# Kernel tuning notes

Measured on AMD Instinct MI355X. Metric: run time of the kernel, lower is better.

The kernel has to match this reference:

```python
import jax, jax.numpy as jnp
import numpy as np

B, N, H_DIM, G_DIM, G_HID, K_CONST = 32, 8192, 256, 256, 512, 64


def setup_inputs() -> dict:
    key = jax.random.key(0)
    k1, k2, k3 = jax.random.split(key, 3)
    hs = jax.random.normal(k1, (B, N, H_DIM), dtype=jnp.float32)
    # Sorted cluster labels 0..K-1, same row for all batch entries (training mode).
    cs_row = ((jnp.arange(N) * K_CONST) // N).astype(jnp.int32)
    cs_o = jnp.tile(cs_row[None, :], (B, 1))
    W1 = jax.random.normal(k2, (H_DIM, G_HID), dtype=jnp.float32) * (1.0 / np.sqrt(H_DIM))
    b1 = jnp.zeros((G_HID,), dtype=jnp.float32)
    W2 = jax.random.normal(k3, (G_HID, G_DIM), dtype=jnp.float32) * (1.0 / np.sqrt(G_HID))
    b2 = jnp.zeros((G_DIM,), dtype=jnp.float32)
    return {"hs": hs, "cs_o": cs_o, "W1": W1, "b1": b1, "W2": W2, "b2": b2,
            "n": N - 1, "K": K_CONST}


def reference(hs, cs_o, W1, b1, W2, b2, n, K):
    # Training mode (cs_is_sample=False): mask points >= n, use row 0 pattern.
    cs = cs_o.at[:, n:].set(-1)
    cs1 = cs[0]  # [N]
    # One-hot cluster membership: [K, N]
    onehot = (cs1[None, :] == jnp.arange(K)[:, None]).astype(hs.dtype)
    # Per-cluster sums H_k: [B, K, h_dim] (single pass, replaces K masked sweeps)
    Hk = jnp.einsum('kn,bnh->bkh', onehot, hs)
    hn = hs[:, n, :]  # [B, h_dim]
    # H = [H_0..H_{K-1}, H_0+h_n..H_{K-1}+h_n, h_n] -> [B, 2K+1, h_dim]
    H = jnp.concatenate([Hk, Hk + hn[:, None, :], hn[:, None, :]], axis=1)
    # g: 2-layer MLP applied rowwise
    gs = jax.nn.relu(H @ W1 + b1) @ W2 + b2  # [B, 2K+1, g_dim]
    # Exclude-sum combine: G[:,k] = sum_{j<K} gs[:,j] - gs[:,k] + gs[:,k+K]
    S = gs[:, :K, :].sum(axis=1)  # [B, g_dim]
    G_front = S[:, None, :] - gs[:, :K, :] + gs[:, K:2 * K, :]
    G_last = (S + gs[:, 2 * K, :])[:, None, :]
    G = jnp.concatenate([G_front, G_last], axis=1)  # [B, K+1, g_dim]
    G_mask = jnp.ones((hs.shape[0], K + 1), dtype=hs.dtype)
    return G, G_mask
```

## Files before the change

### kernel.cpp

```cpp
#include <hip/hip_runtime.h>

#define B_SZ   32
#define N_SZ   8192
#define HDIM   256
#define GHID   512
#define K_CL   64
#define M_ROWS (B_SZ * (2 * K_CL + 1))
#define M_PAD  4224

typedef short v8s __attribute__((ext_vector_type(8)));
typedef float v4f __attribute__((ext_vector_type(4)));

__device__ __forceinline__ unsigned short f32_to_bf16(float f) {
  unsigned int u = __float_as_uint(f);
  u += 0x7FFFu + ((u >> 16) & 1u);
  return (unsigned short)(u >> 16);
}

__device__ __forceinline__ int lower_bound_i(const int* __restrict__ a, int n, int key) {
  int lo = 0, hi = n;
  while (lo < hi) {
    const int mid = (lo + hi) >> 1;
    if (a[mid] < key) lo = mid + 1; else hi = mid;
  }
  return lo;
}

__global__ __launch_bounds__(256) void cluster_sum_kernel(
    const float* __restrict__ hs, const int* __restrict__ cs,
    const int* __restrict__ n_ptr, float* __restrict__ Hk) {
  const int b = blockIdx.x;
  const int k = blockIdx.y;
  const int tid = threadIdx.x;
  const int col = (tid & 63) * 4;
  const int rsub = tid >> 6;
  const int n_val = n_ptr[0];

  const int start = lower_bound_i(cs, N_SZ, k);
  int end = lower_bound_i(cs, N_SZ, k + 1);
  if (end > n_val) end = n_val;

  const float* base = hs + (size_t)b * N_SZ * HDIM + col;

  float4 a0 = make_float4(0.f, 0.f, 0.f, 0.f), a1 = a0, a2 = a0, a3 = a0;
  int r = start + rsub;
  for (; r + 12 < end; r += 16) {
    const float4 v0 = *(const float4*)(base + (size_t)(r) * HDIM);
    const float4 v1 = *(const float4*)(base + (size_t)(r + 4) * HDIM);
    const float4 v2 = *(const float4*)(base + (size_t)(r + 8) * HDIM);
    const float4 v3 = *(const float4*)(base + (size_t)(r + 12) * HDIM);
    a0.x += v0.x; a0.y += v0.y; a0.z += v0.z; a0.w += v0.w;
    a1.x += v1.x; a1.y += v1.y; a1.z += v1.z; a1.w += v1.w;
    a2.x += v2.x; a2.y += v2.y; a2.z += v2.z; a2.w += v2.w;
    a3.x += v3.x; a3.y += v3.y; a3.z += v3.z; a3.w += v3.w;
  }
  for (; r < end; r += 4) {
    const float4 v = *(const float4*)(base + (size_t)r * HDIM);
    a0.x += v.x; a0.y += v.y; a0.z += v.z; a0.w += v.w;
  }
  float4 acc;
  acc.x = (a0.x + a1.x) + (a2.x + a3.x);
  acc.y = (a0.y + a1.y) + (a2.y + a3.y);
  acc.z = (a0.z + a1.z) + (a2.z + a3.z);
  acc.w = (a0.w + a1.w) + (a2.w + a3.w);

  __shared__ float4 red[256];
  red[tid] = acc;
  __syncthreads();
  if (tid < 64) {
    const float4 p0 = red[tid], p1 = red[tid + 64], p2 = red[tid + 128], p3 = red[tid + 192];
    float4 o;
    o.x = (p0.x + p1.x) + (p2.x + p3.x);
    o.y = (p0.y + p1.y) + (p2.y + p3.y);
    o.z = (p0.z + p1.z) + (p2.z + p3.z);
    o.w = (p0.w + p1.w) + (p2.w + p3.w);
    *(float4*)(Hk + ((size_t)b * K_CL + k) * HDIM + tid * 4) = o;
  }
}

__global__ __launch_bounds__(256) void prep_w_kernel(
    const float* __restrict__ W1, const float* __restrict__ W2,
    unsigned short* __restrict__ W1t, unsigned short* __restrict__ W2t) {
  const int idx = blockIdx.x;
  const int tid = threadIdx.x;
  __shared__ float tile[32][33];

  if (idx < 128) {
    const int tr = idx >> 4, tc = idx & 15;
    const int r0 = tid >> 5, c = tid & 31;
#pragma unroll
    for (int p = 0; p < 4; ++p) {
      const int r = p * 8 + r0;
      tile[r][c] = W1[(size_t)(tr * 32 + r) * GHID + tc * 32 + c];
    }
    __syncthreads();
#pragma unroll
    for (int p = 0; p < 4; ++p) {
      const int r = p * 8 + r0;
      W1t[(size_t)(tc * 32 + r) * HDIM + tr * 32 + c] = f32_to_bf16(tile[c][r]);
    }
  } else {
    const int t = idx - 128;
    const int tr = t >> 3, tc = t & 7;
    const int r0 = tid >> 5, c = tid & 31;
#pragma unroll
    for (int p = 0; p < 4; ++p) {
      const int r = p * 8 + r0;
      tile[r][c] = W2[(size_t)(tr * 32 + r) * HDIM + tc * 32 + c];
    }
    __syncthreads();
#pragma unroll
    for (int p = 0; p < 4; ++p) {
      const int r = p * 8 + r0;
      W2t[(size_t)(tc * 32 + r) * GHID + tr * 32 + c] = f32_to_bf16(tile[c][r]);
    }
  }
}

__global__ __launch_bounds__(256) void gemm1_kernel(
    const float* __restrict__ hs, const float* __restrict__ Hk,
    const unsigned short* __restrict__ W1t, const float* __restrict__ bias,
    const int* __restrict__ n_ptr, unsigned short* __restrict__ act) {
  constexpr int BM = 64, BN = 128, BK = 32, LDT = 40;
  constexpr int CT = BN / 16;
  __shared__ unsigned short As[BM * LDT];
  __shared__ unsigned short Bs[BN * LDT];

  const int tid = threadIdx.x;
  const int wave = tid >> 6, lane = tid & 63;
  const int quad = lane >> 4, lr = lane & 15;
  const int row0 = blockIdx.x * BM;
  const int col0 = blockIdx.y * BN;
  const int n_val = n_ptr[0];

  const int sr = tid >> 2;
  const int sk = (tid & 3) * 8;

  const int grow = row0 + sr;
  const int b = grow / 129;
  const int j = grow - b * 129;
  const bool valid = (grow < M_ROWS);
  const bool add_hn = valid && (j >= K_CL);
  const bool use_hk = valid && (j < 2 * K_CL);
  const int jj = (j < K_CL) ? j : (j - K_CL);
  const float* hk_row = Hk + ((size_t)b * K_CL + jj) * HDIM + sk;
  const float* hn_row = hs + ((size_t)b * N_SZ + n_val) * HDIM + sk;

  v4f acc[CT];
#pragma unroll
  for (int ct = 0; ct < CT; ++ct) acc[ct] = (v4f){0.f, 0.f, 0.f, 0.f};

  for (int k0 = 0; k0 < HDIM; k0 += BK) {
    float4 f0 = make_float4(0.f, 0.f, 0.f, 0.f), f1 = f0;
    if (use_hk) {
      f0 = *(const float4*)(hk_row + k0);
      f1 = *(const float4*)(hk_row + k0 + 4);
    }
    if (add_hn) {
      const float4 h0 = *(const float4*)(hn_row + k0);
      const float4 h1 = *(const float4*)(hn_row + k0 + 4);
      f0.x += h0.x; f0.y += h0.y; f0.z += h0.z; f0.w += h0.w;
      f1.x += h1.x; f1.y += h1.y; f1.z += h1.z; f1.w += h1.w;
    }
    unsigned short u[8];
    u[0] = f32_to_bf16(f0.x); u[1] = f32_to_bf16(f0.y);
    u[2] = f32_to_bf16(f0.z); u[3] = f32_to_bf16(f0.w);
    u[4] = f32_to_bf16(f1.x); u[5] = f32_to_bf16(f1.y);
    u[6] = f32_to_bf16(f1.z); u[7] = f32_to_bf16(f1.w);
    *(uint4*)(As + sr * LDT + sk) = *(const uint4*)u;
#pragma unroll
    for (int r = sr; r < BN; r += 64)
      *(uint4*)(Bs + r * LDT + sk) =
          *(const uint4*)(W1t + (size_t)(col0 + r) * HDIM + k0 + sk);
    __syncthreads();

    const v8s a = *(const v8s*)(As + (wave * 16 + lr) * LDT + quad * 8);
#pragma unroll
    for (int ct = 0; ct < CT; ++ct) {
      const v8s bf = *(const v8s*)(Bs + (ct * 16 + lr) * LDT + quad * 8);
      acc[ct] = __builtin_amdgcn_mfma_f32_16x16x32_bf16(a, bf, acc[ct], 0, 0, 0);
    }
    __syncthreads();
  }

#pragma unroll
  for (int ct = 0; ct < CT; ++ct) {
    const int gcol = col0 + ct * 16 + lr;
    const float bv = bias[gcol];
#pragma unroll
    for (int i = 0; i < 4; ++i) {
      const int orow = row0 + wave * 16 + quad * 4 + i;
      act[(size_t)orow * GHID + gcol] = f32_to_bf16(fmaxf(acc[ct][i] + bv, 0.f));
    }
  }
}

__global__ __launch_bounds__(256) void gemm2_kernel(
    const unsigned short* __restrict__ A, const unsigned short* __restrict__ Bt,
    const float* __restrict__ bias, float* __restrict__ C) {
  constexpr int BM = 64, BN = 64, BK = 32, LDT = 40;
  constexpr int CT = BN / 16;
  __shared__ unsigned short As[BM * LDT];
  __shared__ unsigned short Bs[BN * LDT];

  const int tid = threadIdx.x;
  const int wave = tid >> 6, lane = tid & 63;
  const int quad = lane >> 4, lr = lane & 15;
  const int row0 = blockIdx.x * BM;
  const int col0 = blockIdx.y * BN;

  const int sr = tid >> 2;
  const int sk = (tid & 3) * 8;

  v4f acc[CT];
#pragma unroll
  for (int ct = 0; ct < CT; ++ct) acc[ct] = (v4f){0.f, 0.f, 0.f, 0.f};

  for (int k0 = 0; k0 < GHID; k0 += BK) {
    *(uint4*)(As + sr * LDT + sk) =
        *(const uint4*)(A + (size_t)(row0 + sr) * GHID + k0 + sk);
    *(uint4*)(Bs + sr * LDT + sk) =
        *(const uint4*)(Bt + (size_t)(col0 + sr) * GHID + k0 + sk);
    __syncthreads();

    const v8s a = *(const v8s*)(As + (wave * 16 + lr) * LDT + quad * 8);
#pragma unroll
    for (int ct = 0; ct < CT; ++ct) {
      const v8s bf = *(const v8s*)(Bs + (ct * 16 + lr) * LDT + quad * 8);
      acc[ct] = __builtin_amdgcn_mfma_f32_16x16x32_bf16(a, bf, acc[ct], 0, 0, 0);
    }
    __syncthreads();
  }

#pragma unroll
  for (int ct = 0; ct < CT; ++ct) {
    const int gcol = col0 + ct * 16 + lr;
    const float bv = bias[gcol];
#pragma unroll
    for (int i = 0; i < 4; ++i) {
      const int orow = row0 + wave * 16 + quad * 4 + i;
      C[(size_t)orow * HDIM + gcol] = acc[ct][i] + bv;
    }
  }
}

__global__ __launch_bounds__(64) void combine_kernel(
    const float* __restrict__ gs, float* __restrict__ G, float* __restrict__ mask) {
  const int b = blockIdx.x;
  const int h = blockIdx.y * 64 + threadIdx.x;
  const float* g = gs + (size_t)b * (2 * K_CL + 1) * HDIM + h;
  float S = 0.f;
#pragma unroll 8
  for (int k = 0; k < K_CL; ++k) S += g[k * HDIM];
#pragma unroll 4
  for (int k = 0; k < K_CL; ++k) {
    G[((size_t)b * (K_CL + 1) + k) * HDIM + h] = S - g[k * HDIM] + g[(K_CL + k) * HDIM];
  }
  G[((size_t)b * (K_CL + 1) + K_CL) * HDIM + h] = S + g[2 * K_CL * HDIM];
  const int mi = blockIdx.y * 64 + threadIdx.x;
  if (mi < K_CL + 1) mask[b * (K_CL + 1) + mi] = 1.0f;
}

extern "C" void kernel_launch(void* const* d_in, const int* in_sizes, int n_in,
                              void* d_out, int out_size, void* d_ws, size_t ws_size,
                              hipStream_t stream) {
  const float* hs = (const float*)d_in[0];
  const int* cs = (const int*)d_in[1];
  const float* W1 = (const float*)d_in[2];
  const float* b1 = (const float*)d_in[3];
  const float* W2 = (const float*)d_in[4];
  const float* b2 = (const float*)d_in[5];
  const int* n_ptr = (const int*)d_in[6];

  float* G = (float*)d_out;
  float* mask = G + (size_t)B_SZ * (K_CL + 1) * HDIM;

  char* w = (char*)d_ws;
  float* Hk = (float*)w;                     w += (size_t)B_SZ * K_CL * HDIM * 4;
  unsigned short* W1t = (unsigned short*)w;  w += (size_t)GHID * HDIM * 2;
  unsigned short* W2t = (unsigned short*)w;  w += (size_t)HDIM * GHID * 2;
  unsigned short* act = (unsigned short*)w;  w += (size_t)M_PAD * GHID * 2;
  float* gs = (float*)w;

  cluster_sum_kernel<<<dim3(B_SZ, K_CL), 256, 0, stream>>>(hs, cs, n_ptr, Hk);
  prep_w_kernel<<<256, 256, 0, stream>>>(W1, W2, W1t, W2t);
  gemm1_kernel<<<dim3(M_PAD / 64, GHID / 128), 256, 0, stream>>>(
      hs, Hk, W1t, b1, n_ptr, act);
  gemm2_kernel<<<dim3(M_PAD / 64, HDIM / 64), 256, 0, stream>>>(act, W2t, b2, gs);
  combine_kernel<<<dim3(B_SZ, HDIM / 64), 64, 0, stream>>>(gs, G, mask);
}
```

Baseline: 408.9 us.

## Fuse both MLP GEMMs into one kernel and merge weight prep with cluster sum

Combines the cluster-sum and weight transpose/convert kernels into one launch, and fuses the two GEMM layers into a single kernel that keeps the ReLU activations in shared memory. This removes the activation round-trip through global memory and two kernel launches. In exchange, the fused MLP runs only 132 blocks with heavy LDS use, which lowers parallelism on the GPU.

Measured after the change: 400.2 us. 1.02x faster.

```diff
diff --git a/kernel.cpp b/kernel.cpp
--- a/kernel.cpp
+++ b/kernel.cpp
@@ -26,220 +26,224 @@
   return lo;
 }
 
-__global__ __launch_bounds__(256) void cluster_sum_kernel(
+__global__ __launch_bounds__(256) void sum_prep_kernel(
     const float* __restrict__ hs, const int* __restrict__ cs,
-    const int* __restrict__ n_ptr, float* __restrict__ Hk) {
-  const int b = blockIdx.x;
-  const int k = blockIdx.y;
-  const int tid = threadIdx.x;
-  const int col = (tid & 63) * 4;
-  const int rsub = tid >> 6;
-  const int n_val = n_ptr[0];
-
-  const int start = lower_bound_i(cs, N_SZ, k);
-  int end = lower_bound_i(cs, N_SZ, k + 1);
-  if (end > n_val) end = n_val;
-
-  const float* base = hs + (size_t)b * N_SZ * HDIM + col;
-
-  float4 a0 = make_float4(0.f, 0.f, 0.f, 0.f), a1 = a0, a2 = a0, a3 = a0;
-  int r = start + rsub;
-  for (; r + 12 < end; r += 16) {
-    const float4 v0 = *(const float4*)(base + (size_t)(r) * HDIM);
-    const float4 v1 = *(const float4*)(base + (size_t)(r + 4) * HDIM);
-    const float4 v2 = *(const float4*)(base + (size_t)(r + 8) * HDIM);
-    const float4 v3 = *(const float4*)(base + (size_t)(r + 12) * HDIM);
-    a0.x += v0.x; a0.y += v0.y; a0.z += v0.z; a0.w += v0.w;
-    a1.x += v1.x; a1.y += v1.y; a1.z += v1.z; a1.w += v1.w;
-    a2.x += v2.x; a2.y += v2.y; a2.z += v2.z; a2.w += v2.w;
-    a3.x += v3.x; a3.y += v3.y; a3.z += v3.z; a3.w += v3.w;
-  }
-  for (; r < end; r += 4) {
-    const float4 v = *(const float4*)(base + (size_t)r * HDIM);
-    a0.x += v.x; a0.y += v.y; a0.z += v.z; a0.w += v.w;
-  }
-  float4 acc;
-  acc.x = (a0.x + a1.x) + (a2.x + a3.x);
-  acc.y = (a0.y + a1.y) + (a2.y + a3.y);
-  acc.z = (a0.z + a1.z) + (a2.z + a3.z);
-  acc.w = (a0.w + a1.w) + (a2.w + a3.w);
-
-  __shared__ float4 red[256];
-  red[tid] = acc;
-  __syncthreads();
-  if (tid < 64) {
-    const float4 p0 = red[tid], p1 = red[tid + 64], p2 = red[tid + 128], p3 = red[tid + 192];
-    float4 o;
-    o.x = (p0.x + p1.x) + (p2.x + p3.x);
-    o.y = (p0.y + p1.y) + (p2.y + p3.y);
-    o.z = (p0.z + p1.z) + (p2.z + p3.z);
-    o.w = (p0.w + p1.w) + (p2.w + p3.w);
-    *(float4*)(Hk + ((size_t)b * K_CL + k) * HDIM + tid * 4) = o;
-  }
-}
-
-__global__ __launch_bounds__(256) void prep_w_kernel(
+    const int* __restrict__ n_ptr, float* __restrict__ Hk,
     const float* __restrict__ W1, const float* __restrict__ W2,
     unsigned short* __restrict__ W1t, unsigned short* __restrict__ W2t) {
-  const int idx = blockIdx.x;
+  __shared__ float4 red[256];
+  __shared__ float tile[32][33];
+  const int bid = blockIdx.x;
   const int tid = threadIdx.x;
-  __shared__ float tile[32][33];
-
-  if (idx < 128) {
-    const int tr = idx >> 4, tc = idx & 15;
-    const int r0 = tid >> 5, c = tid & 31;
-#pragma unroll
-    for (int p = 0; p < 4; ++p) {
-      const int r = p * 8 + r0;
-      tile[r][c] = W1[(size_t)(tr * 32 + r) * GHID + tc * 32 + c];
-    }
-    __syncthreads();
-#pragma unroll
-    for (int p = 0; p < 4; ++p) {
-      const int r = p * 8 + r0;
-      W1t[(size_t)(tc * 32 + r) * HDIM + tr * 32 + c] = f32_to_bf16(tile[c][r]);
+
+  if (bid < B_SZ * K_CL) {
+    const int b = bid >> 6;
+    const int k = bid & 63;
+    const int col = (tid & 63) * 4;
+    const int rsub = tid >> 6;
+    const int n_val = n_ptr[0];
+
+    const int start = lower_bound_i(cs, N_SZ, k);
+    int end = lower_bound_i(cs, N_SZ, k + 1);
+    if (end > n_val) end = n_val;
+
+    const float* base = hs + (size_t)b * N_SZ * HDIM + col;
+
+    float4 a0 = make_float4(0.f, 0.f, 0.f, 0.f), a1 = a0, a2 = a0, a3 = a0;
+    int r = start + rsub;
+    for (; r + 12 < end; r += 16) {
+      const float4 v0 = *(const float4*)(base + (size_t)(r) * HDIM);
+      const float4 v1 = *(const float4*)(base + (size_t)(r + 4) * HDIM);
+      const float4 v2 = *(const float4*)(base + (size_t)(r + 8) * HDIM);
+      const float4 v3 = *(const float4*)(base + (size_t)(r + 12) * HDIM);
+      a0.x += v0.x; a0.y += v0.y; a0.z += v0.z; a0.w += v0.w;
+      a1.x += v1.x; a1.y += v1.y; a1.z += v1.z; a1.w += v1.w;
+      a2.x += v2.x; a2.y += v2.y; a2.z += v2.z; a2.w += v2.w;
+      a3.x += v3.x; a3.y += v3.y; a3.z += v3.z; a3.w += v3.w;
+    }
+    for (; r < end; r += 4) {
+      const float4 v = *(const float4*)(base + (size_t)r * HDIM);
+      a0.x += v.x; a0.y += v.y; a0.z += v.z; a0.w += v.w;
+    }
+    float4 acc;
+    acc.x = (a0.x + a1.x) + (a2.x + a3.x);
+    acc.y = (a0.y + a1.y) + (a2.y + a3.y);
+    acc.z = (a0.z + a1.z) + (a2.z + a3.z);
+    acc.w = (a0.w + a1.w) + (a2.w + a3.w);
+
+    red[tid] = acc;
+    __syncthreads();
+    if (tid < 64) {
+      const float4 p0 = red[tid], p1 = red[tid + 64], p2 = red[tid + 128], p3 = red[tid + 192];
+      float4 o;
+      o.x = (p0.x + p1.x) + (p2.x + p3.x);
+      o.y = (p0.y + p1.y) + (p2.y + p3.y);
+      o.z = (p0.z + p1.z) + (p2.z + p3.z);
+      o.w = (p0.w + p1.w) + (p2.w + p3.w);
+      *(float4*)(Hk + ((size_t)b * K_CL + k) * HDIM + tid * 4) = o;
     }
   } else {
-    const int t = idx - 128;
-    const int tr = t >> 3, tc = t & 7;
-    const int r0 = tid >> 5, c = tid & 31;
-#pragma unroll
-    for (int p = 0; p < 4; ++p) {
-      const int r = p * 8 + r0;
-      tile[r][c] = W2[(size_t)(tr * 32 + r) * HDIM + tc * 32 + c];
-    }
-    __syncthreads();
-#pragma unroll
-    for (int p = 0; p < 4; ++p) {
-      const int r = p * 8 + r0;
-      W2t[(size_t)(tc * 32 + r) * GHID + tr * 32 + c] = f32_to_bf16(tile[c][r]);
-    }
-  }
-}
-
-__global__ __launch_bounds__(256) void gemm1_kernel(
+    const int idx = bid - B_SZ * K_CL;
+    if (idx < 128) {
+      const int tr = idx >> 4, tc = idx & 15;
+      const int r0 = tid >> 5, c = tid & 31;
+#pragma unroll
+      for (int p = 0; p < 4; ++p) {
+        const int r = p * 8 + r0;
+        tile[r][c] = W1[(size_t)(tr * 32 + r) * GHID + tc * 32 + c];
+      }
+      __syncthreads();
+#pragma unroll
+      for (int p = 0; p < 4; ++p) {
+        const int r = p * 8 + r0;
+        W1t[(size_t)(tc * 32 + r) * HDIM + tr * 32 + c] = f32_to_bf16(tile[c][r]);
+      }
+    } else {
+      const int t = idx - 128;
+      const int tr = t >> 3, tc = t & 7;
+      const int r0 = tid >> 5, c = tid & 31;
+#pragma unroll
+      for (int p = 0; p < 4; ++p) {
+        const int r = p * 8 + r0;
+        tile[r][c] = W2[(size_t)(tr * 32 + r) * HDIM + tc * 32 + c];
+      }
+      __syncthreads();
+#pragma unroll
+      for (int p = 0; p < 4; ++p) {
+        const int r = p * 8 + r0;
+        W2t[(size_t)(tc * 32 + r) * GHID + tr * 32 + c] = f32_to_bf16(tile[c][r]);
+      }
+    }
+  }
+}
+
+__global__ __launch_bounds__(256) void mlp_kernel(
     const float* __restrict__ hs, const float* __restrict__ Hk,
-    const unsigned short* __restrict__ W1t, const float* __restrict__ bias,
-    const int* __restrict__ n_ptr, unsigned short* __restrict__ act) {
-  constexpr int BM = 64, BN = 128, BK = 32, LDT = 40;
-  constexpr int CT = BN / 16;
-  __shared__ unsigned short As[BM * LDT];
-  __shared__ unsigned short Bs[BN * LDT];
+    const unsigned short* __restrict__ W1t, const float* __restrict__ b1,
+    const unsigned short* __restrict__ W2t, const float* __restrict__ b2,
+    const int* __restrict__ n_ptr, float* __restrict__ gs) {
+  constexpr int LDT = 40;
+  constexpr int LDT2 = 72;
+  constexpr int LDA = 520;
+  __shared__ unsigned short As[32 * LDT];
+  __shared__ unsigned short Bs[512 * LDT];
+  __shared__ unsigned short Act[32 * LDA];
 
   const int tid = threadIdx.x;
   const int wave = tid >> 6, lane = tid & 63;
   const int quad = lane >> 4, lr = lane & 15;
-  const int row0 = blockIdx.x * BM;
-  const int col0 = blockIdx.y * BN;
+  const int row0 = blockIdx.x * 32;
   const int n_val = n_ptr[0];
 
-  const int sr = tid >> 2;
-  const int sk = (tid & 3) * 8;
-
-  const int grow = row0 + sr;
+  const int ar = tid >> 3;
+  const int ak = (tid & 7) * 4;
+  const int grow = row0 + ar;
   const int b = grow / 129;
   const int j = grow - b * 129;
   const bool valid = (grow < M_ROWS);
   const bool add_hn = valid && (j >= K_CL);
   const bool use_hk = valid && (j < 2 * K_CL);
   const int jj = (j < K_CL) ? j : (j - K_CL);
-  const float* hk_row = Hk + ((size_t)b * K_CL + jj) * HDIM + sk;
-  const float* hn_row = hs + ((size_t)b * N_SZ + n_val) * HDIM + sk;
-
-  v4f acc[CT];
-#pragma unroll
-  for (int ct = 0; ct < CT; ++ct) acc[ct] = (v4f){0.f, 0.f, 0.f, 0.f};
-
-  for (int k0 = 0; k0 < HDIM; k0 += BK) {
-    float4 f0 = make_float4(0.f, 0.f, 0.f, 0.f), f1 = f0;
-    if (use_hk) {
-      f0 = *(const float4*)(hk_row + k0);
-      f1 = *(const float4*)(hk_row + k0 + 4);
-    }
+  const float* hk_row = Hk + ((size_t)b * K_CL + jj) * HDIM + ak;
+  const float* hn_row = hs + ((size_t)b * N_SZ + n_val) * HDIM + ak;
+
+  v4f acc1[2][8];
+#pragma unroll
+  for (int rt = 0; rt < 2; ++rt)
+#pragma unroll
+    for (int cf = 0; cf < 8; ++cf) acc1[rt][cf] = (v4f){0.f, 0.f, 0.f, 0.f};
+
+  const int brr = tid >> 2;
+  const int bkk = (tid & 3) * 8;
+
+  for (int k0 = 0; k0 < HDIM; k0 += 32) {
+    float4 f = make_float4(0.f, 0.f, 0.f, 0.f);
+    if (use_hk) f = *(const float4*)(hk_row + k0);
     if (add_hn) {
-      const float4 h0 = *(const float4*)(hn_row + k0);
-      const float4 h1 = *(const float4*)(hn_row + k0 + 4);
-      f0.x += h0.x; f0.y += h0.y; f0.z += h0.z; f0.w += h0.w;
-      f1.x += h1.x; f1.y += h1.y; f1.z += h1.z; f1.w += h1.w;
-    }
-    unsigned short u[8];
-    u[0] = f32_to_bf16(f0.x); u[1] = f32_to_bf16(f0.y);
-    u[2] = f32_to_bf16(f0.z); u[3] = f32_to_bf16(f0.w);
-    u[4] = f32_to_bf16(f1.x); u[5] = f32_to_bf16(f1.y);
-    u[6] = f32_to_bf16(f1.z); u[7] = f32_to_bf16(f1.w);
-    *(uint4*)(As + sr * LDT + sk) = *(const uint4*)u;
-#pragma unroll
-    for (int r = sr; r < BN; r += 64)
-      *(uint4*)(Bs + r * LDT + sk) =
-          *(const uint4*)(W1t + (size_t)(col0 + r) * HDIM + k0 + sk);
-    __syncthreads();
-
-    const v8s a = *(const v8s*)(As + (wave * 16 + lr) * LDT + quad * 8);
-#pragma unroll
-    for (int ct = 0; ct < CT; ++ct) {
-      const v8s bf = *(const v8s*)(Bs + (ct * 16 + lr) * LDT + quad * 8);
-      acc[ct] = __builtin_amdgcn_mfma_f32_16x16x32_bf16(a, bf, acc[ct], 0, 0, 0);
-    }
-    __syncthreads();
-  }
-
-#pragma unroll
-  for (int ct = 0; ct < CT; ++ct) {
-    const int gcol = col0 + ct * 16 + lr;
-    const float bv = bias[gcol];
-#pragma unroll
-    for (int i = 0; i < 4; ++i) {
-      const int orow = row0 + wave * 16 + quad * 4 + i;
-      act[(size_t)orow * GHID + gcol] = f32_to_bf16(fmaxf(acc[ct][i] + bv, 0.f));
-    }
-  }
-}
-
-__global__ __launch_bounds__(256) void gemm2_kernel(
-    const unsigned short* __restrict__ A, const unsigned short* __restrict__ Bt,
-    const float* __restrict__ bias, float* __restrict__ C) {
-  constexpr int BM = 64, BN = 64, BK = 32, LDT = 40;
-  constexpr int CT = BN / 16;
-  __shared__ unsigned short As[BM * LDT];
-  __shared__ unsigned short Bs[BN * LDT];
-
-  const int tid = threadIdx.x;
-  const int wave = tid >> 6, lane = tid & 63;
-  const int quad = lane >> 4, lr = lane & 15;
-  const int row0 = blockIdx.x * BM;
-  const int col0 = blockIdx.y * BN;
-
-  const int sr = tid >> 2;
-  const int sk = (tid & 3) * 8;
-
-  v4f acc[CT];
-#pragma unroll
-  for (int ct = 0; ct < CT; ++ct) acc[ct] = (v4f){0.f, 0.f, 0.f, 0.f};
-
-  for (int k0 = 0; k0 < GHID; k0 += BK) {
-    *(uint4*)(As + sr * LDT + sk) =
-        *(const uint4*)(A + (size_t)(row0 + sr) * GHID + k0 + sk);
-    *(uint4*)(Bs + sr * LDT + sk) =
-        *(const uint4*)(Bt + (size_t)(col0 + sr) * GHID + k0 + sk);
-    __syncthreads();
-
-    const v8s a = *(const v8s*)(As + (wave * 16 + lr) * LDT + quad * 8);
-#pragma unroll
-    for (int ct = 0; ct < CT; ++ct) {
-      const v8s bf = *(const v8s*)(Bs + (ct * 16 + lr) * LDT + quad * 8);
-      acc[ct] = __builtin_amdgcn_mfma_f32_16x16x32_bf16(a, bf, acc[ct], 0, 0, 0);
-    }
-    __syncthreads();
-  }
-
-#pragma unroll
-  for (int ct = 0; ct < CT; ++ct) {
-    const int gcol = col0 + ct * 16 + lr;
-    const float bv = bias[gcol];
-#pragma unroll
-    for (int i = 0; i < 4; ++i) {
-      const int orow = row0 + wave * 16 + quad * 4 + i;
-      C[(size_t)orow * HDIM + gcol] = acc[ct][i] + bv;
+      const float4 h = *(const float4*)(hn_row + k0);
+      f.x += h.x; f.y += h.y; f.z += h.z; f.w += h.w;
+    }
+    unsigned short u[4];
+    u[0] = f32_to_bf16(f.x); u[1] = f32_to_bf16(f.y);
+    u[2] = f32_to_bf16(f.z); u[3] = f32_to_bf16(f.w);
+    *(uint2*)(As + ar * LDT + ak) = *(const uint2*)u;
+#pragma unroll
+    for (int p = 0; p < 8; ++p) {
+      *(uint4*)(Bs + (p * 64 + brr) * LDT + bkk) =
+          *(const uint4*)(W1t + (size_t)(p * 64 + brr) * HDIM + k0 + bkk);
+    }
+    __syncthreads();
+
+#pragma unroll
+    for (int rt = 0; rt < 2; ++rt) {
+      const v8s a = *(const v8s*)(As + (rt * 16 + lr) * LDT + quad * 8);
+#pragma unroll
+      for (int cf = 0; cf < 8; ++cf) {
+        const v8s bf = *(const v8s*)(Bs + (wave * 128 + cf * 16 + lr) * LDT + quad * 8);
+        acc1[rt][cf] = __builtin_amdgcn_mfma_f32_16x16x32_bf16(a, bf, acc1[rt][cf], 0, 0, 0);
+      }
+    }
+    __syncthreads();
+  }
+
+#pragma unroll
+  for (int rt = 0; rt < 2; ++rt) {
+#pragma unroll
+    for (int cf = 0; cf < 8; ++cf) {
+      const int col = wave * 128 + cf * 16 + lr;
+      const float bv = b1[col];
+#pragma unroll
+      for (int i = 0; i < 4; ++i) {
+        const int row = rt * 16 + quad * 4 + i;
+        Act[row * LDA + col] = f32_to_bf16(fmaxf(acc1[rt][cf][i] + bv, 0.f));
+      }
+    }
+  }
+  __syncthreads();
+
+  v4f acc2[2][4];
+#pragma unroll
+  for (int rt = 0; rt < 2; ++rt)
+#pragma unroll
+    for (int cf = 0; cf < 4; ++cf) acc2[rt][cf] = (v4f){0.f, 0.f, 0.f, 0.f};
+
+  const int br2 = tid >> 3;
+  const int bk2 = (tid & 7) * 8;
+
+  for (int k0 = 0; k0 < GHID; k0 += 64) {
+#pragma unroll
+    for (int p = 0; p < 8; ++p) {
+      *(uint4*)(Bs + (p * 32 + br2) * LDT2 + bk2) =
+          *(const uint4*)(W2t + (size_t)(p * 32 + br2) * GHID + k0 + bk2);
+    }
+    __syncthreads();
+
+#pragma unroll
+    for (int kk = 0; kk < 64; kk += 32) {
+#pragma unroll
+      for (int rt = 0; rt < 2; ++rt) {
+        const v8s a = *(const v8s*)(Act + (rt * 16 + lr) * LDA + k0 + kk + quad * 8);
+#pragma unroll
+        for (int cf = 0; cf < 4; ++cf) {
+          const v8s bf = *(const v8s*)(Bs + (wave * 64 + cf * 16 + lr) * LDT2 + kk + quad * 8);
+          acc2[rt][cf] = __builtin_amdgcn_mfma_f32_16x16x32_bf16(a, bf, acc2[rt][cf], 0, 0, 0);
+        }
+      }
+    }
+    __syncthreads();
+  }
+
+#pragma unroll
+  for (int rt = 0; rt < 2; ++rt) {
+#pragma unroll
+    for (int cf = 0; cf < 4; ++cf) {
+      const int col = wave * 64 + cf * 16 + lr;
+      const float bv = b2[col];
+#pragma unroll
+      for (int i = 0; i < 4; ++i) {
+        const int row = row0 + rt * 16 + quad * 4 + i;
+        gs[(size_t)row * HDIM + col] = acc2[rt][cf][i] + bv;
+      }
     }
   }
 }
@@ -279,13 +283,10 @@
   float* Hk = (float*)w;                     w += (size_t)B_SZ * K_CL * HDIM * 4;
   unsigned short* W1t = (unsigned short*)w;  w += (size_t)GHID * HDIM * 2;
   unsigned short* W2t = (unsigned short*)w;  w += (size_t)HDIM * GHID * 2;
-  unsigned short* act = (unsigned short*)w;  w += (size_t)M_PAD * GHID * 2;
   float* gs = (float*)w;
 
-  cluster_sum_kernel<<<dim3(B_SZ, K_CL), 256, 0, stream>>>(hs, cs, n_ptr, Hk);
-  prep_w_kernel<<<256, 256, 0, stream>>>(W1, W2, W1t, W2t);
-  gemm1_kernel<<<dim3(M_PAD / 64, GHID / 128), 256, 0, stream>>>(
-      hs, Hk, W1t, b1, n_ptr, act);
-  gemm2_kernel<<<dim3(M_PAD / 64, HDIM / 64), 256, 0, stream>>>(act, W2t, b2, gs);
+  sum_prep_kernel<<<B_SZ * K_CL + 256, 256, 0, stream>>>(
+      hs, cs, n_ptr, Hk, W1, W2, W1t, W2t);
+  mlp_kernel<<<M_PAD / 32, 256, 0, stream>>>(hs, Hk, W1t, b1, W2t, b2, n_ptr, gs);
   combine_kernel<<<dim3(B_SZ, HDIM / 64), 64, 0, stream>>>(gs, G, mask);
 }
```
